# Kernel tuning notes

Hardware: AMD Instinct MI355X
Metric: run time of the kernel (lower is better)

The kernel has to match this reference:

```python
import jax, jax.numpy as jnp
import numpy as np

CLS_NUM = 2
SCALE = 8.0
NO_OBJ_SCALE = 1.0
EPS = 1e-7


def setup_inputs() -> dict:
    key = jax.random.key(0)
    k1, k2, k3, k4, k5, k6 = jax.random.split(key, 6)
    B, C, H, W, N = 8, CLS_NUM, 512, 512, 160
    predict = jax.random.normal(k1, (B, C, H, W), dtype=jnp.float32)
    b = jax.random.randint(k2, (N,), 0, B).astype(jnp.float32)
    c = jax.random.randint(k3, (N,), 0, C).astype(jnp.float32)
    cxy = jax.random.uniform(k4, (N, 2), minval=0.0, maxval=H * SCALE)
    wh = jax.random.uniform(k5, (N, 2), minval=64.0, maxval=256.0)
    ang = jax.random.uniform(k6, (N, 1), minval=-np.pi, maxval=np.pi)
    targets = jnp.concatenate([b[:, None], c[:, None], cxy, wh, ang], axis=1).astype(jnp.float32)
    return {"predict": predict, "targets": targets}


def _forward(predict, targets):
    B, C, H, W = predict.shape
    pred = jnp.transpose(predict, (0, 2, 3, 1))          # [B,H,W,C]
    conf_all = jax.nn.sigmoid(pred)
    heatmap = jnp.max(conf_all, axis=-1)                 # [B,H,W]

    bid = targets[:, 0].astype(jnp.int32)                # [N] batch ids
    cid = targets[:, 1].astype(jnp.int32)                # [N] class ids
    cx = targets[:, 2] / SCALE
    cy = targets[:, 3] / SCALE
    w = targets[:, 4] / SCALE
    h = targets[:, 5] / SCALE
    ang = targets[:, 6]
    cos, sin = jnp.cos(ang), jnp.sin(ang)
    # rotate box center into the rotated frame (same math as render_map)
    x = cx * cos + cy * sin
    y = -cx * sin + cy * cos
    x3, x4 = x - h / 2, x + h / 2
    y3, y4 = y - w / 2, y + w / 2
    x1, x2 = x3 - 0.5, x4 + 0.5
    y1, y2 = y3 - 0.5, y4 + 0.5

    gx = jnp.arange(W, dtype=jnp.float32)[None, :] + 0.5  # [1,W] -> broadcasts to [H,W]
    gy = jnp.arange(H, dtype=jnp.float32)[:, None] + 0.5  # [H,1]
    vx = cos[:, None, None] * gx + sin[:, None, None] * gy   # [N,H,W]
    vy = -sin[:, None, None] * gx + cos[:, None, None] * gy  # [N,H,W]

    def box_mask(lo_x, hi_x, lo_y, hi_y):
        return ((lo_x[:, None, None] <= vx) & (vx <= hi_x[:, None, None]) &
                (lo_y[:, None, None] <= vy) & (vy <= hi_y[:, None, None]))

    inner = box_mask(x3, x4, y3, y4)  # obj region, [N,H,W]
    outer = box_mask(x1, x2, y1, y2)  # expanded region (clears noobj)

    loss = jnp.float32(0.0)
    for cls in range(CLS_NUM):
        sel = (cid == cls)[:, None, None]
        obj_cnt = jax.ops.segment_sum((inner & sel).astype(jnp.float32), bid, num_segments=B)
        out_cnt = jax.ops.segment_sum((outer & sel).astype(jnp.float32), bid, num_segments=B)
        obj_mask = obj_cnt > 0            # [B,H,W]
        noobj_mask = out_cnt <= 0         # starts at 1, zeroed inside any expanded box
        conf_c = jnp.clip(conf_all[..., cls], EPS, 1.0 - EPS)
        n_obj = jnp.sum(obj_mask)
        n_noobj = jnp.sum(noobj_mask)
        # BCE with target 1 on obj cells, target 0 on noobj cells (tconf == obj mask)
        loss_obj = -jnp.sum(jnp.where(obj_mask, jnp.log(conf_c), 0.0)) / jnp.maximum(n_obj, 1)
        loss_noobj = -jnp.sum(jnp.where(noobj_mask, jnp.log(1.0 - conf_c), 0.0)) / jnp.maximum(n_noobj, 1)
        loss = loss + jnp.where(n_obj > 0, loss_obj + NO_OBJ_SCALE * loss_noobj, 0.0)
    return loss, heatmap


def reference(predict, targets):
    return _forward(predict, targets)
```

## Files before the change

kernel.cpp:

```cpp
#include <hip/hip_runtime.h>
#include <math.h>

#define CLS 2
#define BATCH 8
#define HH 512
#define WW 512
#define INV_SCALE 0.125f
#define LOGEPS -16.118095651f

#define NB 512
#define TSTRIDE 192


__global__ __launch_bounds__(256) void heatmap_prep(
    const float* __restrict__ targets, int nT, double* __restrict__ gsum,
    int* __restrict__ gcnt, int* __restrict__ bcnt, float* __restrict__ tdat)
{
    __shared__ int s_b[BATCH];
    const int t = threadIdx.x;
    if (t < BATCH) s_b[t] = 0;
    for (int q = t; q < 4 * NB; q += 256) { gsum[q] = 0.0; gcnt[q] = 0; }
    __syncthreads();
    if (t < nT) {
        const float* tp = targets + t * 7;
        const int b = (int)tp[0];
        const float cs = cosf(tp[6]), sn = sinf(tp[6]);
        const float cx = tp[2] * INV_SCALE, cy = tp[3] * INV_SCALE;
        const float w_ = tp[4] * INV_SCALE, h_ = tp[5] * INV_SCALE;
        const float x = cx * cs + cy * sn;
        const float y = -cx * sn + cy * cs;
        const int slot = atomicAdd(&s_b[b], 1);
        float* tbp = tdat + b * (7 * TSTRIDE);
        tbp[0 * TSTRIDE + slot] = cs;
        tbp[1 * TSTRIDE + slot] = sn;
        tbp[2 * TSTRIDE + slot] = x - 0.5f * h_;
        tbp[3 * TSTRIDE + slot] = x + 0.5f * h_;
        tbp[4 * TSTRIDE + slot] = y - 0.5f * w_;
        tbp[5 * TSTRIDE + slot] = y + 0.5f * w_;
        ((int*)tbp)[6 * TSTRIDE + slot] = (int)tp[1];
    }
    __syncthreads();
    if (t < BATCH) bcnt[t] = s_b[t];
}

__global__ __launch_bounds__(256) void heatmap_main(
    const float* __restrict__ predict, float* __restrict__ out,
    double* __restrict__ gsum, int* __restrict__ gcnt,
    const int* __restrict__ bcnt, const float* __restrict__ tdat)
{
    const int wid = threadIdx.x >> 6;
    const int l   = threadIdx.x & 63;
    const int sidx = blockIdx.x * 4 + wid;
    const int blockPix = sidx * 256;
    const int b  = blockPix >> 18;
    const int i  = (blockPix >> 9) & (HH - 1);
    const int j0 = blockPix & (WW - 1);
    const float gy = (float)i + 0.5f;

    const int j = j0 + 4 * l;
    const float gxb = (float)j + 0.5f;

    const int nb = bcnt[b];
    const float* tbp = tdat + b * (7 * TSTRIDE);

    int objm[4] = {0, 0, 0, 0}, outm[4] = {0, 0, 0, 0};

    for (int base = 0; base < nb; base += 64) {
        const int t = base + l;
        float cs = 0.f, sn = 0.f, x3 = 0.f, x4 = 0.f, y3 = 0.f, y4 = 0.f;
        int cid = 0;
        bool acc = false;
        if (t < nb) {
            cs = tbp[0 * TSTRIDE + t]; sn = tbp[1 * TSTRIDE + t];
            x3 = tbp[2 * TSTRIDE + t]; x4 = tbp[3 * TSTRIDE + t];
            y3 = tbp[4 * TSTRIDE + t]; y4 = tbp[5 * TSTRIDE + t];
            cid = ((const int*)tbp)[6 * TSTRIDE + t];
            const float gxl = (float)j0 + 0.5f, gxh = (float)j0 + 255.5f;
            const float a1 = cs * gxl + sn * gy, a2 = cs * gxh + sn * gy;
            const float b1 = -sn * gxl + cs * gy, b2 = -sn * gxh + cs * gy;
            const float vxlo = fminf(a1, a2), vxhi = fmaxf(a1, a2);
            const float vylo = fminf(b1, b2), vyhi = fmaxf(b1, b2);
            const float M = 0.51f;
            acc = (vxhi >= x3 - M) & (vxlo <= x4 + M) &
                  (vyhi >= y3 - M) & (vylo <= y4 + M);
        }
        unsigned long long bal = __ballot(acc);
        while (bal) {
            const int n = __builtin_ctzll(bal);
            bal &= bal - 1;
            const float ccs = __shfl(cs, n), csn = __shfl(sn, n);
            const float cx3 = __shfl(x3, n), cx4 = __shfl(x4, n);
            const float cy3 = __shfl(y3, n), cy4 = __shfl(y4, n);
            const int cbit = 1 << __shfl(cid, n);
            float vx = ccs * gxb + csn * gy;
            float vy = -csn * gxb + ccs * gy;
            #pragma unroll
            for (int k = 0; k < 4; ++k) {
                const bool in_  = (cx3 <= vx) & (vx <= cx4) &
                                  (cy3 <= vy) & (vy <= cy4);
                const bool out_ = (cx3 - 0.5f <= vx) & (vx <= cx4 + 0.5f) &
                                  (cy3 - 0.5f <= vy) & (vy <= cy4 + 0.5f);
                if (in_)  objm[k] |= cbit;
                if (out_) outm[k] |= cbit;
                vx += ccs; vy -= csn;
            }
        }
    }

    const int pbase = (b * CLS * HH + i) * WW + j;
    const float4 P0 = *(const float4*)(predict + pbase);
    const float4 P1 = *(const float4*)(predict + pbase + HH * WW);

    float so0 = 0.f, so1 = 0.f, sq0 = 0.f, sq1 = 0.f;
    int c_obj0 = 0, c_obj1 = 0, c_no0 = 0, c_no1 = 0;
    float hm[4];
    #pragma unroll
    for (int k = 0; k < 4; ++k) {
        const float p0 = (&P0.x)[k], p1 = (&P1.x)[k];
        const float t0 = __expf(p0), t1 = __expf(p1);
        const float l0n = -__logf(1.0f + t0);
        const float l1n = -__logf(1.0f + t1);
        const float lc0 = fmaxf(p0 + l0n, LOGEPS);
        const float lc1 = fmaxf(p1 + l1n, LOGEPS);
        const float l0c = fmaxf(l0n, LOGEPS);
        const float l1c = fmaxf(l1n, LOGEPS);
        const float tm = fmaxf(t0, t1);
        hm[k] = tm * __builtin_amdgcn_rcpf(1.0f + tm);
        const int om = objm[k], um = outm[k];
        if (om & 1) { so0 += lc0; ++c_obj0; }
        if (om & 2) { so1 += lc1; ++c_obj1; }
        if (!(um & 1)) { sq0 += l0c; ++c_no0; }
        if (!(um & 2)) { sq1 += l1c; ++c_no1; }
    }

    float* ho = out + 1 + (b * HH + i) * WW + j;
    ho[0] = hm[0]; ho[1] = hm[1]; ho[2] = hm[2]; ho[3] = hm[3];

    const unsigned long long anyobj =
        __ballot((objm[0] | objm[1] | objm[2] | objm[3]) != 0);
    int pc = (c_no0 & 0xffff) | (c_no1 << 16);
    #pragma unroll
    for (int off = 32; off >= 1; off >>= 1) {
        sq0 += __shfl_down(sq0, off);
        sq1 += __shfl_down(sq1, off);
        pc  += __shfl_down(pc, off);
    }
    int po = 0;
    if (anyobj) {
        po = (c_obj0 & 0xffff) | (c_obj1 << 16);
        #pragma unroll
        for (int off = 32; off >= 1; off >>= 1) {
            so0 += __shfl_down(so0, off);
            so1 += __shfl_down(so1, off);
            po  += __shfl_down(po, off);
        }
    }
    if (l == 0) {
        const int bkt = sidx & (NB - 1);
        atomicAdd(&gsum[2 * NB + bkt], (double)sq0);
        atomicAdd(&gsum[3 * NB + bkt], (double)sq1);
        atomicAdd(&gcnt[2 * NB + bkt], pc & 0xffff);
        atomicAdd(&gcnt[3 * NB + bkt], pc >> 16);
        if (anyobj) {
            const int o0 = po & 0xffff, o1 = po >> 16;
            if (o0) { atomicAdd(&gsum[0 * NB + bkt], (double)so0);
                      atomicAdd(&gcnt[0 * NB + bkt], o0); }
            if (o1) { atomicAdd(&gsum[1 * NB + bkt], (double)so1);
                      atomicAdd(&gcnt[1 * NB + bkt], o1); }
        }
    }
}

__global__ __launch_bounds__(512) void heatmap_finalize(
    const double* __restrict__ gsum, const int* __restrict__ gcnt,
    float* __restrict__ out)
{
    const int t = threadIdx.x;
    double f[4]; int c[4];
    #pragma unroll
    for (int q = 0; q < 4; ++q) { f[q] = gsum[q * NB + t]; c[q] = gcnt[q * NB + t]; }

    #pragma unroll
    for (int off = 32; off >= 1; off >>= 1) {
        #pragma unroll
        for (int q = 0; q < 4; ++q) {
            f[q] += __shfl_down(f[q], off);
            c[q] += __shfl_down(c[q], off);
        }
    }

    __shared__ double sf[8][4];
    __shared__ int    si[8][4];
    const int wv = t >> 6, ln = t & 63;
    if (ln == 0) {
        #pragma unroll
        for (int q = 0; q < 4; ++q) { sf[wv][q] = f[q]; si[wv][q] = c[q]; }
    }
    __syncthreads();
    if (t == 0) {
        double F[4] = {0, 0, 0, 0}; int C[4] = {0, 0, 0, 0};
        for (int w = 0; w < 8; ++w)
            #pragma unroll
            for (int q = 0; q < 4; ++q) { F[q] += sf[w][q]; C[q] += si[w][q]; }
        float loss = 0.0f;
        #pragma unroll
        for (int cls = 0; cls < CLS; ++cls) {
            const int no = C[cls];
            const int nn = C[2 + cls];
            if (no > 0) {
                const float lo  = -(float)F[cls]     / (float)(no > 1 ? no : 1);
                const float ln_ = -(float)F[2 + cls] / (float)(nn > 1 ? nn : 1);
                loss += lo + ln_;
            }
        }
        out[0] = loss;
    }
}

extern "C" void kernel_launch(void* const* d_in, const int* in_sizes, int n_in,
                              void* d_out, int out_size, void* d_ws, size_t ws_size,
                              hipStream_t stream) {
    const float* predict = (const float*)d_in[0];
    const float* targets = (const float*)d_in[1];
    const int nT = in_sizes[1] / 7;
    float* out = (float*)d_out;
    char* ws = (char*)d_ws;
    double* gsum = (double*)ws;
    int* gcnt = (int*)(ws + 16384);
    int* bcnt = (int*)(ws + 24576);
    float* tdat = (float*)(ws + 24608);

    heatmap_prep<<<1, 256, 0, stream>>>(targets, nT, gsum, gcnt, bcnt, tdat);
    const int nstrips = BATCH * HH * WW / 256;
    heatmap_main<<<nstrips / 4, 256, 0, stream>>>(predict, out, gsum, gcnt,
                                                  bcnt, tdat);
    heatmap_finalize<<<1, 512, 0, stream>>>(gsum, gcnt, out);
}
```

Baseline: 80.96 us.

## Fuse target prep into main kernel and replace atomics with per-strip partials

```diff
diff --git a/kernel.cpp b/kernel.cpp
--- a/kernel.cpp
+++ b/kernel.cpp
@@ -8,45 +8,13 @@
 #define INV_SCALE 0.125f
 #define LOGEPS -16.118095651f
 
-#define NB 512
-#define TSTRIDE 192
-
-
-__global__ __launch_bounds__(256) void heatmap_prep(
-    const float* __restrict__ targets, int nT, double* __restrict__ gsum,
-    int* __restrict__ gcnt, int* __restrict__ bcnt, float* __restrict__ tdat)
-{
-    __shared__ int s_b[BATCH];
-    const int t = threadIdx.x;
-    if (t < BATCH) s_b[t] = 0;
-    for (int q = t; q < 4 * NB; q += 256) { gsum[q] = 0.0; gcnt[q] = 0; }
-    __syncthreads();
-    if (t < nT) {
-        const float* tp = targets + t * 7;
-        const int b = (int)tp[0];
-        const float cs = cosf(tp[6]), sn = sinf(tp[6]);
-        const float cx = tp[2] * INV_SCALE, cy = tp[3] * INV_SCALE;
-        const float w_ = tp[4] * INV_SCALE, h_ = tp[5] * INV_SCALE;
-        const float x = cx * cs + cy * sn;
-        const float y = -cx * sn + cy * cs;
-        const int slot = atomicAdd(&s_b[b], 1);
-        float* tbp = tdat + b * (7 * TSTRIDE);
-        tbp[0 * TSTRIDE + slot] = cs;
-        tbp[1 * TSTRIDE + slot] = sn;
-        tbp[2 * TSTRIDE + slot] = x - 0.5f * h_;
-        tbp[3 * TSTRIDE + slot] = x + 0.5f * h_;
-        tbp[4 * TSTRIDE + slot] = y - 0.5f * w_;
-        tbp[5 * TSTRIDE + slot] = y + 0.5f * w_;
-        ((int*)tbp)[6 * TSTRIDE + slot] = (int)tp[1];
-    }
-    __syncthreads();
-    if (t < BATCH) bcnt[t] = s_b[t];
-}
+#define NSTRIP 8192
+
 
 __global__ __launch_bounds__(256) void heatmap_main(
-    const float* __restrict__ predict, float* __restrict__ out,
-    double* __restrict__ gsum, int* __restrict__ gcnt,
-    const int* __restrict__ bcnt, const float* __restrict__ tdat)
+    const float* __restrict__ predict, const float* __restrict__ targets,
+    int nT, float* __restrict__ out, float* __restrict__ pf,
+    int* __restrict__ pi)
 {
     const int wid = threadIdx.x >> 6;
     const int l   = threadIdx.x & 63;
@@ -60,28 +28,31 @@
     const int j = j0 + 4 * l;
     const float gxb = (float)j + 0.5f;
 
-    const int nb = bcnt[b];
-    const float* tbp = tdat + b * (7 * TSTRIDE);
-
     int objm[4] = {0, 0, 0, 0}, outm[4] = {0, 0, 0, 0};
 
-    for (int base = 0; base < nb; base += 64) {
+    for (int base = 0; base < nT; base += 64) {
         const int t = base + l;
         float cs = 0.f, sn = 0.f, x3 = 0.f, x4 = 0.f, y3 = 0.f, y4 = 0.f;
         int cid = 0;
         bool acc = false;
-        if (t < nb) {
-            cs = tbp[0 * TSTRIDE + t]; sn = tbp[1 * TSTRIDE + t];
-            x3 = tbp[2 * TSTRIDE + t]; x4 = tbp[3 * TSTRIDE + t];
-            y3 = tbp[4 * TSTRIDE + t]; y4 = tbp[5 * TSTRIDE + t];
-            cid = ((const int*)tbp)[6 * TSTRIDE + t];
+        if (t < nT) {
+            const float* tp = targets + t * 7;
+            const int tb = (int)tp[0];
+            cid = (int)tp[1];
+            const float cx = tp[2] * INV_SCALE, cy = tp[3] * INV_SCALE;
+            const float w_ = tp[4] * INV_SCALE, h_ = tp[5] * INV_SCALE;
+            cs = cosf(tp[6]); sn = sinf(tp[6]);
+            const float x = cx * cs + cy * sn;
+            const float y = -cx * sn + cy * cs;
+            x3 = x - 0.5f * h_; x4 = x + 0.5f * h_;
+            y3 = y - 0.5f * w_; y4 = y + 0.5f * w_;
             const float gxl = (float)j0 + 0.5f, gxh = (float)j0 + 255.5f;
             const float a1 = cs * gxl + sn * gy, a2 = cs * gxh + sn * gy;
             const float b1 = -sn * gxl + cs * gy, b2 = -sn * gxh + cs * gy;
             const float vxlo = fminf(a1, a2), vxhi = fmaxf(a1, a2);
             const float vylo = fminf(b1, b2), vyhi = fmaxf(b1, b2);
             const float M = 0.51f;
-            acc = (vxhi >= x3 - M) & (vxlo <= x4 + M) &
+            acc = (tb == b) & (vxhi >= x3 - M) & (vxlo <= x4 + M) &
                   (vyhi >= y3 - M) & (vylo <= y4 + M);
         }
         unsigned long long bal = __ballot(acc);
@@ -156,30 +127,32 @@
         }
     }
     if (l == 0) {
-        const int bkt = sidx & (NB - 1);
-        atomicAdd(&gsum[2 * NB + bkt], (double)sq0);
-        atomicAdd(&gsum[3 * NB + bkt], (double)sq1);
-        atomicAdd(&gcnt[2 * NB + bkt], pc & 0xffff);
-        atomicAdd(&gcnt[3 * NB + bkt], pc >> 16);
-        if (anyobj) {
-            const int o0 = po & 0xffff, o1 = po >> 16;
-            if (o0) { atomicAdd(&gsum[0 * NB + bkt], (double)so0);
-                      atomicAdd(&gcnt[0 * NB + bkt], o0); }
-            if (o1) { atomicAdd(&gsum[1 * NB + bkt], (double)so1);
-                      atomicAdd(&gcnt[1 * NB + bkt], o1); }
-        }
+        pf[0 * NSTRIP + sidx] = so0;
+        pf[1 * NSTRIP + sidx] = so1;
+        pf[2 * NSTRIP + sidx] = sq0;
+        pf[3 * NSTRIP + sidx] = sq1;
+        pi[0 * NSTRIP + sidx] = po;
+        pi[1 * NSTRIP + sidx] = pc;
     }
 }
 
-__global__ __launch_bounds__(512) void heatmap_finalize(
-    const double* __restrict__ gsum, const int* __restrict__ gcnt,
+__global__ __launch_bounds__(1024) void heatmap_finalize(
+    const float* __restrict__ pf, const int* __restrict__ pi,
     float* __restrict__ out)
 {
     const int t = threadIdx.x;
-    double f[4]; int c[4];
-    #pragma unroll
-    for (int q = 0; q < 4; ++q) { f[q] = gsum[q * NB + t]; c[q] = gcnt[q * NB + t]; }
-
+    double f[4] = {0, 0, 0, 0};
+    int c[4] = {0, 0, 0, 0};
+    for (int s = t; s < NSTRIP; s += 1024) {
+        f[0] += pf[0 * NSTRIP + s];
+        f[1] += pf[1 * NSTRIP + s];
+        f[2] += pf[2 * NSTRIP + s];
+        f[3] += pf[3 * NSTRIP + s];
+        const int po = pi[0 * NSTRIP + s];
+        const int pc = pi[1 * NSTRIP + s];
+        c[0] += po & 0xffff; c[1] += po >> 16;
+        c[2] += pc & 0xffff; c[3] += pc >> 16;
+    }
     #pragma unroll
     for (int off = 32; off >= 1; off >>= 1) {
         #pragma unroll
@@ -188,9 +161,8 @@
             c[q] += __shfl_down(c[q], off);
         }
     }
-
-    __shared__ double sf[8][4];
-    __shared__ int    si[8][4];
+    __shared__ double sf[16][4];
+    __shared__ int    si[16][4];
     const int wv = t >> 6, ln = t & 63;
     if (ln == 0) {
         #pragma unroll
@@ -199,7 +171,7 @@
     __syncthreads();
     if (t == 0) {
         double F[4] = {0, 0, 0, 0}; int C[4] = {0, 0, 0, 0};
-        for (int w = 0; w < 8; ++w)
+        for (int w = 0; w < 16; ++w)
             #pragma unroll
             for (int q = 0; q < 4; ++q) { F[q] += sf[w][q]; C[q] += si[w][q]; }
         float loss = 0.0f;
@@ -225,14 +197,10 @@
     const int nT = in_sizes[1] / 7;
     float* out = (float*)d_out;
     char* ws = (char*)d_ws;
-    double* gsum = (double*)ws;
-    int* gcnt = (int*)(ws + 16384);
-    int* bcnt = (int*)(ws + 24576);
-    float* tdat = (float*)(ws + 24608);
-
-    heatmap_prep<<<1, 256, 0, stream>>>(targets, nT, gsum, gcnt, bcnt, tdat);
-    const int nstrips = BATCH * HH * WW / 256;
-    heatmap_main<<<nstrips / 4, 256, 0, stream>>>(predict, out, gsum, gcnt,
-                                                  bcnt, tdat);
-    heatmap_finalize<<<1, 512, 0, stream>>>(gsum, gcnt, out);
+    float* pf = (float*)ws;
+    int* pi = (int*)(ws + 4 * NSTRIP * sizeof(float));
+
+    heatmap_main<<<NSTRIP / 4, 256, 0, stream>>>(predict, targets, nT, out,
+                                                 pf, pi);
+    heatmap_finalize<<<1, 1024, 0, stream>>>(pf, pi, out);
 }
```

Result: slower. 84.65 us (+4.6%).
